# Performance work log

Hardware: AMD Instinct MI355X
Metric: run time of the kernel (lower is better)

Reference implementation:

```python
import jax, jax.numpy as jnp
import numpy as np

N_NODES = 50000   # gates in the circuit batch
N_HOPS = 100000   # number of k-hop cones
MAX_PI = 8        # max PIs per hop (padded, masked via stats == -1)
D = 128           # token_emb / hidden
D_FF = 4 * D      # cls_head hidden width (512)
TT = 64           # max_tt_len -> logits width
LN_EPS = 1e-5


def setup_inputs() -> dict:
    key = jax.random.key(0)
    ks = jax.random.split(key, 8)
    hf = jax.random.normal(ks[0], (N_NODES, D), jnp.float32)
    all_hop_pi = jax.random.randint(ks[1], (N_HOPS, MAX_PI), 0, N_NODES)
    # stats in {-1, 0, 1}; -1 marks an invalid (padded) PI slot
    all_hop_pi_stats = jax.random.randint(ks[2], (N_HOPS, MAX_PI), 0, 3) - 1
    all_hop_po = jax.random.randint(ks[3], (N_HOPS,), 0, N_NODES)
    w_q = jax.random.normal(ks[4], (D,), jnp.float32) / np.sqrt(D)
    W1 = jax.random.normal(ks[5], (D, D_FF), jnp.float32) / np.sqrt(D)
    b1 = jnp.zeros((D_FF,), jnp.float32)
    gamma = jnp.ones((D_FF,), jnp.float32)
    beta = jnp.zeros((D_FF,), jnp.float32)
    W2 = jax.random.normal(ks[6], (D_FF, TT), jnp.float32) / np.sqrt(D_FF)
    b2 = jnp.zeros((TT,), jnp.float32)
    return {
        'hf': hf, 'w_q': w_q, 'W1': W1, 'b1': b1, 'gamma': gamma,
        'beta': beta, 'W2': W2, 'b2': b2,
        'all_hop_pi': all_hop_pi, 'all_hop_pi_stats': all_hop_pi_stats,
        'all_hop_po': all_hop_po,
    }


def reference(hf, w_q, W1, b1, gamma, beta, W2, b2,
              all_hop_pi, all_hop_pi_stats, all_hop_po):
    # Per-hop gather: valid PI embeddings + PO embedding -> [H, P+1, D]
    pi_tok = hf[all_hop_pi]                       # [H, P, D]
    po_tok = hf[all_hop_po][:, None, :]           # [H, 1, D]
    tokens = jnp.concatenate([pi_tok, po_tok], axis=1)
    valid = jnp.concatenate(
        [all_hop_pi_stats != -1,
         jnp.ones((all_hop_po.shape[0], 1), bool)], axis=1)  # [H, P+1]
    # tf_Pooling: masked single-query attention pooling over the ragged set
    scores = jnp.einsum('hpd,d->hp', tokens, w_q) / jnp.sqrt(jnp.float32(D))
    scores = jnp.where(valid, scores, jnp.float32(-1e30))
    attn = jax.nn.softmax(scores, axis=-1)
    hop_hf = jnp.einsum('hp,hpd->hd', attn, tokens)  # [H, D]
    # cls_head: Linear(D, 4D) -> ReLU -> LayerNorm(4D) -> Linear(4D, TT)
    h = jax.nn.relu(hop_hf @ W1 + b1)
    mu = jnp.mean(h, axis=-1, keepdims=True)
    var = jnp.var(h, axis=-1, keepdims=True)
    h = (h - mu) * jax.lax.rsqrt(var + LN_EPS) * gamma + beta
    logits = h @ W2 + b2                           # [H, TT]
    return logits
```

## Files before the change

### kernel.cpp

```cpp
#include <hip/hip_runtime.h>
#include <hip/hip_bf16.h>
#include <math.h>

#define DIM 128
#define DFF 512
#define TTW 64
#define NPI 8
#define NTOK 9
#define TILE_H 32

typedef __attribute__((ext_vector_type(8))) short short8;
typedef __attribute__((ext_vector_type(4))) float float4v;

__device__ __forceinline__ float bf16lo_f32(unsigned u) {
    union { unsigned u; float f; } v; v.u = u << 16;
    return v.f;
}
__device__ __forceinline__ float bf16hi_f32(unsigned u) {
    union { unsigned u; float f; } v; v.u = u & 0xffff0000u;
    return v.f;
}
__device__ __forceinline__ unsigned pk_bf16(float a, float b) {
    __hip_bfloat162 h = __float22bfloat162_rn(float2{a, b});
    union { __hip_bfloat162 h; unsigned u; } cv; cv.h = h;
    return cv.u;
}

__global__ __launch_bounds__(256)
void prep_k(const float* __restrict__ hf, const float* __restrict__ W1,
            const float* __restrict__ W2,
            unsigned short* __restrict__ hf2, unsigned short* __restrict__ w1t,
            unsigned short* __restrict__ w2t,
            int n_hf, int B_HF)
{
    __shared__ float tile[32][33];
    const int b = blockIdx.x, t = threadIdx.x;
    if (b < B_HF) {
        int i = (b * 256 + t) * 8;
        if (i < n_hf) {
            float4v v0 = *(const float4v*)(hf + i);
            float4v v1 = *(const float4v*)(hf + i + 4);
            uint4 o;
            o.x = pk_bf16(v0[0], v0[1]);
            o.y = pk_bf16(v0[2], v0[3]);
            o.z = pk_bf16(v1[0], v1[1]);
            o.w = pk_bf16(v1[2], v1[3]);
            *(uint4*)(hf2 + i) = o;
        }
    } else if (b < B_HF + 64) {
        const int tb = b - B_HF;
        const int r0 = (tb & 3) * 32, c0 = (tb >> 2) * 32;
        const int ty = t >> 3, tx = t & 7;
        *(float4v*)&tile[ty][tx * 4] = *(const float4v*)(W1 + (r0 + ty) * DFF + c0 + tx * 4);
        __syncthreads();
        uint2 o;
        o.x = pk_bf16(tile[tx * 4 + 0][ty], tile[tx * 4 + 1][ty]);
        o.y = pk_bf16(tile[tx * 4 + 2][ty], tile[tx * 4 + 3][ty]);
        *(uint2*)(w1t + (c0 + ty) * DIM + r0 + tx * 4) = o;
    } else {
        const int tb = b - B_HF - 64;
        const int r0 = (tb & 15) * 32, c0 = (tb >> 4) * 32;
        const int ty = t >> 3, tx = t & 7;
        *(float4v*)&tile[ty][tx * 4] = *(const float4v*)(W2 + (r0 + ty) * TTW + c0 + tx * 4);
        __syncthreads();
        uint2 o;
        o.x = pk_bf16(tile[tx * 4 + 0][ty], tile[tx * 4 + 1][ty]);
        o.y = pk_bf16(tile[tx * 4 + 2][ty], tile[tx * 4 + 3][ty]);
        *(uint2*)(w2t + (c0 + ty) * DFF + r0 + tx * 4) = o;
    }
}

__global__ __launch_bounds__(256, 4)
void fused_k(const unsigned short* __restrict__ hf2,
             const float* __restrict__ w_q,
             const int* __restrict__ pi,
             const int* __restrict__ stats,
             const int* __restrict__ po,
             const unsigned short* __restrict__ w1t,
             const float* __restrict__ b1,
             const float* __restrict__ gamma,
             const float* __restrict__ beta,
             const unsigned short* __restrict__ w2t,
             const float* __restrict__ b2,
             float* __restrict__ out,
             int H)
{
    __shared__ __align__(16) unsigned short Apool[TILE_H][DIM + 8];
    __shared__ __align__(16) unsigned short Hsm[TILE_H][256 + 8];
    __shared__ float part[2][16][4][2];

    const int t    = threadIdx.x;
    const int lane = t & 63;
    const int w    = t >> 6;
    const int row  = lane & 15;
    const int quad = lane >> 4;
    const int hop0 = blockIdx.x * TILE_H;

    {
        const int g = t >> 5, l = t & 31;
        const float4v wq4 = *(const float4v*)(w_q + l * 4);

        int idxs[4][NTOK];
        unsigned vm[4];
        #pragma unroll
        for (int it = 0; it < 4; ++it) {
            int hop = hop0 + g + it * 8;
            if (hop >= H) hop = H - 1;
            int4 p0 = *(const int4*)(pi + hop * NPI);
            int4 p1 = *(const int4*)(pi + hop * NPI + 4);
            int4 s0 = *(const int4*)(stats + hop * NPI);
            int4 s1 = *(const int4*)(stats + hop * NPI + 4);
            idxs[it][0] = p0.x; idxs[it][1] = p0.y;
            idxs[it][2] = p0.z; idxs[it][3] = p0.w;
            idxs[it][4] = p1.x; idxs[it][5] = p1.y;
            idxs[it][6] = p1.z; idxs[it][7] = p1.w;
            idxs[it][8] = po[hop];
            vm[it] = (s0.x != -1 ? 1u   : 0u) | (s0.y != -1 ? 2u   : 0u)
                   | (s0.z != -1 ? 4u   : 0u) | (s0.w != -1 ? 8u   : 0u)
                   | (s1.x != -1 ? 16u  : 0u) | (s1.y != -1 ? 32u  : 0u)
                   | (s1.z != -1 ? 64u  : 0u) | (s1.w != -1 ? 128u : 0u)
                   | 256u;
        }
        uint2 tu[4][NTOK];
        #pragma unroll
        for (int it = 0; it < 4; ++it)
            #pragma unroll
            for (int p = 0; p < NTOK; ++p)
                tu[it][p] = *(const uint2*)(hf2 + (size_t)idxs[it][p] * DIM + l * 4);

        #pragma unroll
        for (int it = 0; it < 4; ++it) {
            const int hl = g + it * 8;
            float tok[NTOK][4];
            #pragma unroll
            for (int p = 0; p < NTOK; ++p) {
                tok[p][0] = bf16lo_f32(tu[it][p].x);
                tok[p][1] = bf16hi_f32(tu[it][p].x);
                tok[p][2] = bf16lo_f32(tu[it][p].y);
                tok[p][3] = bf16hi_f32(tu[it][p].y);
            }
            float sc[NTOK];
            #pragma unroll
            for (int p = 0; p < NTOK; ++p)
                sc[p] = tok[p][0]*wq4[0] + tok[p][1]*wq4[1]
                      + tok[p][2]*wq4[2] + tok[p][3]*wq4[3];
            #pragma unroll
            for (int m = 1; m < 32; m <<= 1) {
                #pragma unroll
                for (int p = 0; p < NTOK; ++p) sc[p] += __shfl_xor(sc[p], m);
            }
            const float isd = 0.08838834764831845f;
            float mx = -1e30f;
            #pragma unroll
            for (int p = 0; p < NTOK; ++p) {
                sc[p] = ((vm[it] >> p) & 1u) ? sc[p] * isd : -1e30f;
                mx = fmaxf(mx, sc[p]);
            }
            float se = 0.f;
            #pragma unroll
            for (int p = 0; p < NTOK; ++p) { sc[p] = __expf(sc[p] - mx); se += sc[p]; }
            const float inv = 1.f / se;
            float a0=0.f, a1=0.f, a2=0.f, a3=0.f;
            #pragma unroll
            for (int p = 0; p < NTOK; ++p) {
                float a = sc[p] * inv;
                a0 += a * tok[p][0]; a1 += a * tok[p][1];
                a2 += a * tok[p][2]; a3 += a * tok[p][3];
            }
            uint2 o;
            o.x = pk_bf16(a0, a1);
            o.y = pk_bf16(a2, a3);
            *(uint2*)&Apool[hl][l * 4] = o;
        }
    }
    __syncthreads();

    float4v acc[8][2];
    #pragma unroll
    for (int mt = 0; mt < 8; ++mt) {
        acc[mt][0] = (float4v){0.f, 0.f, 0.f, 0.f};
        acc[mt][1] = (float4v){0.f, 0.f, 0.f, 0.f};
    }
    {
        short8 bfr[2][4];
        #pragma unroll
        for (int ks = 0; ks < 4; ++ks) {
            const int k0 = ks * 32 + quad * 8;
            #pragma unroll
            for (int ht = 0; ht < 2; ++ht)
                bfr[ht][ks] = *(const short8*)&Apool[ht * 16 + row][k0];
        }
        #pragma unroll
        for (int mt = 0; mt < 8; ++mt) {
            const unsigned short* wrow = w1t + (size_t)(mt * 64 + w * 16 + row) * DIM;
            #pragma unroll
            for (int ks = 0; ks < 4; ++ks) {
                short8 afr = *(const short8*)(wrow + ks * 32 + quad * 8);
                acc[mt][0] = __builtin_amdgcn_mfma_f32_16x16x32_bf16(afr, bfr[0][ks], acc[mt][0], 0, 0, 0);
                acc[mt][1] = __builtin_amdgcn_mfma_f32_16x16x32_bf16(afr, bfr[1][ks], acc[mt][1], 0, 0, 0);
            }
        }
    }
    float sum0 = 0.f, ssq0 = 0.f, sum1 = 0.f, ssq1 = 0.f;
    #pragma unroll
    for (int mt = 0; mt < 8; ++mt) {
        const int nb = mt * 64 + w * 16 + quad * 4;
        const float4v bias = *(const float4v*)(b1 + nb);
        #pragma unroll
        for (int r = 0; r < 4; ++r) {
            float v0 = fmaxf(acc[mt][0][r] + bias[r], 0.f);
            float v1 = fmaxf(acc[mt][1][r] + bias[r], 0.f);
            acc[mt][0][r] = v0;  sum0 += v0;  ssq0 += v0 * v0;
            acc[mt][1][r] = v1;  sum1 += v1;  ssq1 += v1 * v1;
        }
    }
    #pragma unroll
    for (int m = 16; m <= 32; m <<= 1) {
        sum0 += __shfl_xor(sum0, m);  ssq0 += __shfl_xor(ssq0, m);
        sum1 += __shfl_xor(sum1, m);  ssq1 += __shfl_xor(ssq1, m);
    }
    if (lane < 16) {
        part[0][row][w][0] = sum0;  part[0][row][w][1] = ssq0;
        part[1][row][w][0] = sum1;  part[1][row][w][1] = ssq1;
    }
    __syncthreads();
    float mu[2], rs[2];
    #pragma unroll
    for (int ht = 0; ht < 2; ++ht) {
        float S = 0.f, Q = 0.f;
        #pragma unroll
        for (int ww = 0; ww < 4; ++ww) {
            S += part[ht][row][ww][0];
            Q += part[ht][row][ww][1];
        }
        const float invn = 1.f / (float)DFF;
        mu[ht] = S * invn;
        float var = Q * invn - mu[ht] * mu[ht];
        rs[ht] = rsqrtf(var + 1e-5f);
    }
    uint2 pk[8][2];
    #pragma unroll
    for (int mt = 0; mt < 8; ++mt) {
        const int nb = mt * 64 + w * 16 + quad * 4;
        const float4v g4  = *(const float4v*)(gamma + nb);
        const float4v be4 = *(const float4v*)(beta + nb);
        #pragma unroll
        for (int ht = 0; ht < 2; ++ht) {
            float o[4];
            #pragma unroll
            for (int r = 0; r < 4; ++r) {
                float tg = rs[ht] * g4[r];
                o[r] = acc[mt][ht][r] * tg + (be4[r] - mu[ht] * tg);
            }
            pk[mt][ht].x = pk_bf16(o[0], o[1]);
            pk[mt][ht].y = pk_bf16(o[2], o[3]);
        }
    }
    {
        float4v acc2[2];
        acc2[0] = (float4v){0.f,0.f,0.f,0.f};
        acc2[1] = (float4v){0.f,0.f,0.f,0.f};
        #pragma unroll
        for (int c = 0; c < 2; ++c) {
            #pragma unroll
            for (int m4 = 0; m4 < 4; ++m4) {
                const int col = m4 * 64 + w * 16 + quad * 4;
                *(uint2*)&Hsm[0 * 16 + row][col] = pk[c * 4 + m4][0];
                *(uint2*)&Hsm[1 * 16 + row][col] = pk[c * 4 + m4][1];
            }
            __syncthreads();
            const unsigned short* w2row = w2t + (size_t)(w * 16 + row) * DFF + c * 256;
            #pragma unroll
            for (int ks = 0; ks < 8; ++ks) {
                const int k0 = ks * 32 + quad * 8;
                short8 bfr = *(const short8*)(w2row + k0);
                #pragma unroll
                for (int mt = 0; mt < 2; ++mt) {
                    short8 afr = *(const short8*)&Hsm[mt * 16 + row][k0];
                    acc2[mt] = __builtin_amdgcn_mfma_f32_16x16x32_bf16(
                        afr, bfr, acc2[mt], 0, 0, 0);
                }
            }
            if (c == 0) __syncthreads();
        }
        const float bb = b2[w * 16 + row];
        #pragma unroll
        for (int mt = 0; mt < 2; ++mt) {
            #pragma unroll
            for (int r = 0; r < 4; ++r) {
                int hop = hop0 + mt * 16 + quad * 4 + r;
                if (hop < H)
                    out[(size_t)hop * TTW + w * 16 + row] = acc2[mt][r] + bb;
            }
        }
    }
}

extern "C" void kernel_launch(void* const* d_in, const int* in_sizes, int n_in,
                              void* d_out, int out_size, void* d_ws, size_t ws_size,
                              hipStream_t stream) {
    const float* hf    = (const float*)d_in[0];
    const float* w_q   = (const float*)d_in[1];
    const float* W1    = (const float*)d_in[2];
    const float* b1    = (const float*)d_in[3];
    const float* gamma = (const float*)d_in[4];
    const float* beta  = (const float*)d_in[5];
    const float* W2    = (const float*)d_in[6];
    const float* b2    = (const float*)d_in[7];
    const int* pi      = (const int*)d_in[8];
    const int* stats   = (const int*)d_in[9];
    const int* po      = (const int*)d_in[10];
    float* out         = (float*)d_out;

    const int n_hf = in_sizes[0];
    const int H    = in_sizes[10];
    const int ntiles = (H + TILE_H - 1) / TILE_H;

    char* ws = (char*)d_ws;
    unsigned short* w1t = (unsigned short*)ws;
    unsigned short* w2t = (unsigned short*)(ws + 131072);
    unsigned short* hf2 = (unsigned short*)(ws + 196608);

    const int B_HF = (n_hf + 2047) / 2048;
    hipLaunchKernelGGL(prep_k, dim3(B_HF + 96), dim3(256), 0, stream,
                       hf, W1, W2, hf2, w1t, w2t, n_hf, B_HF);
    hipLaunchKernelGGL(fused_k, dim3(ntiles), dim3(256), 0, stream,
                       hf2, w_q, pi, stats, po, w1t, b1, gamma, beta, w2t, b2, out, H);
}
```

Measured before the change: 235.1 us.

## Fold LayerNorm affine into W2 and apply mean/rstd after second GEMM

Gamma is folded into the transposed W2 during preprocessing, along with per-output constants C1 = gamma·W2 and C2 = b2 + beta·W2. The fused kernel then packs the raw ReLU output to bf16 straight away and applies mean and rstd as a scalar correction on the 64-wide logits instead of normalizing all 512 hidden values. This removes the gamma/beta loads and the per-element normalize pass, and lets pk be produced in the first loop, freeing registers from acc. The risks are extra bf16 rounding error because un-normalized activations and gamma-scaled weights are quantized, a single-block serial 512-step loop in prep, and a lower launch_bounds occupancy hint (4 to 3).

```diff
diff --git a/kernel.cpp b/kernel.cpp
--- a/kernel.cpp
+++ b/kernel.cpp
@@ -28,9 +28,11 @@
 
 __global__ __launch_bounds__(256)
 void prep_k(const float* __restrict__ hf, const float* __restrict__ W1,
-            const float* __restrict__ W2,
+            const float* __restrict__ W2, const float* __restrict__ gamma,
+            const float* __restrict__ beta, const float* __restrict__ b2,
             unsigned short* __restrict__ hf2, unsigned short* __restrict__ w1t,
-            unsigned short* __restrict__ w2t,
+            unsigned short* __restrict__ w2g,
+            float* __restrict__ C1, float* __restrict__ C2,
             int n_hf, int B_HF)
 {
     __shared__ float tile[32][33];
@@ -57,20 +59,34 @@
         o.x = pk_bf16(tile[tx * 4 + 0][ty], tile[tx * 4 + 1][ty]);
         o.y = pk_bf16(tile[tx * 4 + 2][ty], tile[tx * 4 + 3][ty]);
         *(uint2*)(w1t + (c0 + ty) * DIM + r0 + tx * 4) = o;
-    } else {
+    } else if (b < B_HF + 96) {
         const int tb = b - B_HF - 64;
         const int r0 = (tb & 15) * 32, c0 = (tb >> 4) * 32;
         const int ty = t >> 3, tx = t & 7;
-        *(float4v*)&tile[ty][tx * 4] = *(const float4v*)(W2 + (r0 + ty) * TTW + c0 + tx * 4);
+        const float g = gamma[r0 + ty];
+        float4v v = *(const float4v*)(W2 + (r0 + ty) * TTW + c0 + tx * 4);
+        v[0] *= g; v[1] *= g; v[2] *= g; v[3] *= g;
+        *(float4v*)&tile[ty][tx * 4] = v;
         __syncthreads();
         uint2 o;
         o.x = pk_bf16(tile[tx * 4 + 0][ty], tile[tx * 4 + 1][ty]);
         o.y = pk_bf16(tile[tx * 4 + 2][ty], tile[tx * 4 + 3][ty]);
-        *(uint2*)(w2t + (c0 + ty) * DFF + r0 + tx * 4) = o;
-    }
-}
-
-__global__ __launch_bounds__(256, 4)
+        *(uint2*)(w2g + (c0 + ty) * DFF + r0 + tx * 4) = o;
+    } else {
+        if (t < TTW) {
+            float c1 = 0.f, c2 = 0.f;
+            for (int k = 0; k < DFF; ++k) {
+                float w = W2[k * TTW + t];
+                c1 += gamma[k] * w;
+                c2 += beta[k] * w;
+            }
+            C1[t] = c1;
+            C2[t] = b2[t] + c2;
+        }
+    }
+}
+
+__global__ __launch_bounds__(256, 3)
 void fused_k(const unsigned short* __restrict__ hf2,
              const float* __restrict__ w_q,
              const int* __restrict__ pi,
@@ -78,16 +94,16 @@
              const int* __restrict__ po,
              const unsigned short* __restrict__ w1t,
              const float* __restrict__ b1,
-             const float* __restrict__ gamma,
-             const float* __restrict__ beta,
-             const unsigned short* __restrict__ w2t,
-             const float* __restrict__ b2,
+             const unsigned short* __restrict__ w2g,
+             const float* __restrict__ C1,
+             const float* __restrict__ C2,
              float* __restrict__ out,
              int H)
 {
     __shared__ __align__(16) unsigned short Apool[TILE_H][DIM + 8];
     __shared__ __align__(16) unsigned short Hsm[TILE_H][256 + 8];
     __shared__ float part[2][16][4][2];
+    __shared__ float2 mursm[TILE_H];
 
     const int t    = threadIdx.x;
     const int lane = t & 63;
@@ -202,17 +218,21 @@
         }
     }
     float sum0 = 0.f, ssq0 = 0.f, sum1 = 0.f, ssq1 = 0.f;
+    uint2 pk[8][2];
     #pragma unroll
     for (int mt = 0; mt < 8; ++mt) {
         const int nb = mt * 64 + w * 16 + quad * 4;
         const float4v bias = *(const float4v*)(b1 + nb);
+        float o0[4], o1[4];
         #pragma unroll
         for (int r = 0; r < 4; ++r) {
-            float v0 = fmaxf(acc[mt][0][r] + bias[r], 0.f);
-            float v1 = fmaxf(acc[mt][1][r] + bias[r], 0.f);
-            acc[mt][0][r] = v0;  sum0 += v0;  ssq0 += v0 * v0;
-            acc[mt][1][r] = v1;  sum1 += v1;  ssq1 += v1 * v1;
-        }
+            o0[r] = fmaxf(acc[mt][0][r] + bias[r], 0.f);
+            o1[r] = fmaxf(acc[mt][1][r] + bias[r], 0.f);
+            sum0 += o0[r];  ssq0 += o0[r] * o0[r];
+            sum1 += o1[r];  ssq1 += o1[r] * o1[r];
+        }
+        pk[mt][0].x = pk_bf16(o0[0], o0[1]);  pk[mt][0].y = pk_bf16(o0[2], o0[3]);
+        pk[mt][1].x = pk_bf16(o1[0], o1[1]);  pk[mt][1].y = pk_bf16(o1[2], o1[3]);
     }
     #pragma unroll
     for (int m = 16; m <= 32; m <<= 1) {
@@ -224,36 +244,24 @@
         part[1][row][w][0] = sum1;  part[1][row][w][1] = ssq1;
     }
     __syncthreads();
-    float mu[2], rs[2];
-    #pragma unroll
-    for (int ht = 0; ht < 2; ++ht) {
-        float S = 0.f, Q = 0.f;
-        #pragma unroll
-        for (int ww = 0; ww < 4; ++ww) {
-            S += part[ht][row][ww][0];
-            Q += part[ht][row][ww][1];
-        }
+    {
         const float invn = 1.f / (float)DFF;
-        mu[ht] = S * invn;
-        float var = Q * invn - mu[ht] * mu[ht];
-        rs[ht] = rsqrtf(var + 1e-5f);
-    }
-    uint2 pk[8][2];
-    #pragma unroll
-    for (int mt = 0; mt < 8; ++mt) {
-        const int nb = mt * 64 + w * 16 + quad * 4;
-        const float4v g4  = *(const float4v*)(gamma + nb);
-        const float4v be4 = *(const float4v*)(beta + nb);
-        #pragma unroll
-        for (int ht = 0; ht < 2; ++ht) {
-            float o[4];
-            #pragma unroll
-            for (int r = 0; r < 4; ++r) {
-                float tg = rs[ht] * g4[r];
-                o[r] = acc[mt][ht][r] * tg + (be4[r] - mu[ht] * tg);
-            }
-            pk[mt][ht].x = pk_bf16(o[0], o[1]);
-            pk[mt][ht].y = pk_bf16(o[2], o[3]);
+        float mu0, rs0, mu1, rs1;
+        {
+            float S = 0.f, Q = 0.f;
+            #pragma unroll
+            for (int ww = 0; ww < 4; ++ww) { S += part[0][row][ww][0]; Q += part[0][row][ww][1]; }
+            mu0 = S * invn;  rs0 = rsqrtf(Q * invn - mu0 * mu0 + 1e-5f);
+        }
+        {
+            float S = 0.f, Q = 0.f;
+            #pragma unroll
+            for (int ww = 0; ww < 4; ++ww) { S += part[1][row][ww][0]; Q += part[1][row][ww][1]; }
+            mu1 = S * invn;  rs1 = rsqrtf(Q * invn - mu1 * mu1 + 1e-5f);
+        }
+        if (t < 16) {
+            mursm[t]      = float2{mu0, rs0};
+            mursm[16 + t] = float2{mu1, rs1};
         }
     }
     {
@@ -269,7 +277,7 @@
                 *(uint2*)&Hsm[1 * 16 + row][col] = pk[c * 4 + m4][1];
             }
             __syncthreads();
-            const unsigned short* w2row = w2t + (size_t)(w * 16 + row) * DFF + c * 256;
+            const unsigned short* w2row = w2g + (size_t)(w * 16 + row) * DFF + c * 256;
             #pragma unroll
             for (int ks = 0; ks < 8; ++ks) {
                 const int k0 = ks * 32 + quad * 8;
@@ -283,14 +291,19 @@
             }
             if (c == 0) __syncthreads();
         }
-        const float bb = b2[w * 16 + row];
+        const int tt = w * 16 + row;
+        const float c1v = C1[tt];
+        const float c2v = C2[tt];
         #pragma unroll
         for (int mt = 0; mt < 2; ++mt) {
             #pragma unroll
             for (int r = 0; r < 4; ++r) {
-                int hop = hop0 + mt * 16 + quad * 4 + r;
-                if (hop < H)
-                    out[(size_t)hop * TTW + w * 16 + row] = acc2[mt][r] + bb;
+                const int hl = mt * 16 + quad * 4 + r;
+                int hop = hop0 + hl;
+                if (hop < H) {
+                    float2 mr = mursm[hl];
+                    out[(size_t)hop * TTW + tt] = mr.y * (acc2[mt][r] - mr.x * c1v) + c2v;
+                }
             }
         }
     }
@@ -318,12 +331,14 @@
 
     char* ws = (char*)d_ws;
     unsigned short* w1t = (unsigned short*)ws;
-    unsigned short* w2t = (unsigned short*)(ws + 131072);
+    unsigned short* w2g = (unsigned short*)(ws + 131072);
     unsigned short* hf2 = (unsigned short*)(ws + 196608);
+    float* C1 = (float*)(ws + 196608 + (size_t)n_hf * 2);
+    float* C2 = C1 + TTW;
 
     const int B_HF = (n_hf + 2047) / 2048;
-    hipLaunchKernelGGL(prep_k, dim3(B_HF + 96), dim3(256), 0, stream,
-                       hf, W1, W2, hf2, w1t, w2t, n_hf, B_HF);
+    hipLaunchKernelGGL(prep_k, dim3(B_HF + 97), dim3(256), 0, stream,
+                       hf, W1, W2, gamma, beta, b2, hf2, w1t, w2g, C1, C2, n_hf, B_HF);
     hipLaunchKernelGGL(fused_k, dim3(ntiles), dim3(256), 0, stream,
-                       hf2, w_q, pi, stats, po, w1t, b1, gamma, beta, w2t, b2, out, H);
-}
+                       hf2, w_q, pi, stats, po, w1t, b1, w2g, C1, C2, out, H);
+}
```

Measured after the change: 225.6 us. -4.1%, faster.
